# Kernel optimization log

Hardware: AMD Instinct MI355X
Metric: run time of the kernel (lower is better)

The kernel has to match this reference:

```python
import jax, jax.numpy as jnp
import numpy as np
from jax import lax


def setup_inputs() -> dict:
    key = jax.random.key(0)
    k1, k2 = jax.random.split(key)
    B, H, W, C = 8, 32, 32, 512
    N = 16384
    feature_batch = jax.random.normal(k1, (B, H, W, C), dtype=jnp.float32)
    mb = jax.random.normal(k2, (N, C), dtype=jnp.float32)
    return {"feature_batch": feature_batch, "mb": mb, "b": 9}


def reference(feature_batch, mb, b):
    B, H, W, C = feature_batch.shape
    fv = feature_batch.reshape(B * H * W, C)                       # (Q, C)
    sq = (
        jnp.sum(fv * fv, axis=1)[:, None]
        + jnp.sum(mb * mb, axis=1)[None, :]
        - 2.0 * (fv @ mb.T)
    )                                                               # (Q, N)
    sq = jnp.maximum(sq, 0.0)  # guard fp round-off before sqrt
    # smallest-b distances, sorted ascending (top_k of negated values)
    neg_topk = lax.top_k(-sq, b)[0]                                 # (Q, b)
    top_k_dists_squared = -neg_topk
    pixel_scores = jnp.sqrt(top_k_dists_squared[:, 0]).reshape(B, H * W)
    max_idx = jnp.argmax(pixel_scores, axis=1)                      # (B,)
    softmax_args = jnp.sqrt(
        top_k_dists_squared.reshape(B, H * W, b)[jnp.arange(B), max_idx, :]
    )                                                               # (B, b)
    image_scores = softmax_args[:, 0]
    if b > 1:
        image_scores = image_scores * (1.0 - jax.nn.softmax(softmax_args, axis=1)[:, 0])
    pixel_scores = pixel_scores.reshape(B, 1, H, W)
    return pixel_scores, image_scores
```

## Files before the change

kernel.cpp:

```cpp
#include <hip/hip_runtime.h>

typedef unsigned short u16;

#define M_ROWS 8192
#define N_ROWS 16384
#define KDIM   512
#define BM     256
#define BN     256
#define BK     32
#define NCHUNKS 16
#define NPER   (N_ROWS / NCHUNKS)
#define TOPK   9

#define ASZ (BM * BK)
#define BSZ (BN * BK)
#define NTT ((NPER / BN) * (KDIM / BK))

typedef __attribute__((ext_vector_type(8)))  short bf16x8;
typedef __attribute__((ext_vector_type(16))) float f32x16;

__device__ __forceinline__ void gload_lds16(const void* g, void* l) {
  __builtin_amdgcn_global_load_lds(
      (const __attribute__((address_space(1))) void*)g,
      (__attribute__((address_space(3))) void*)l,
      16, 0, 0);
}

__device__ __forceinline__ u16 f2bf(float x) {
  union { float f; unsigned u; } c; c.f = x;
  unsigned u = c.u;
  u += 0x7fffu + ((u >> 16) & 1u);
  return (u16)(u >> 16);
}

__device__ __forceinline__ void topk_update(float v, float* best) {
  if (v < best[TOPK - 1]) {
    #pragma unroll
    for (int i = 0; i < TOPK; ++i) {
      float b = best[i];
      best[i] = fminf(b, v);
      v = fmaxf(b, v);
    }
  }
}

__global__ __launch_bounds__(256) void prep_kernel(
    const float* __restrict__ fv, const float* __restrict__ mb,
    u16* __restrict__ fvb, u16* __restrict__ mbb,
    float* __restrict__ nf, float* __restrict__ nm_perm)
{
  int idx = blockIdx.x * 4 + (threadIdx.x >> 6);
  int l = threadIdx.x & 63;
  const float* src; u16* dst;
  if (idx < M_ROWS) {
    src = fv + (size_t)idx * KDIM; dst = fvb + (size_t)idx * KDIM;
  } else {
    int r = idx - M_ROWS;
    src = mb + (size_t)r * KDIM; dst = mbb + (size_t)r * KDIM;
  }
  float4 x0 = ((const float4*)src)[2 * l];
  float4 x1 = ((const float4*)src)[2 * l + 1];
  float s = x0.x * x0.x + x0.y * x0.y + x0.z * x0.z + x0.w * x0.w
          + x1.x * x1.x + x1.y * x1.y + x1.z * x1.z + x1.w * x1.w;
  uint4 o;
  o.x = (unsigned)f2bf(x0.x) | ((unsigned)f2bf(x0.y) << 16);
  o.y = (unsigned)f2bf(x0.z) | ((unsigned)f2bf(x0.w) << 16);
  o.z = (unsigned)f2bf(x1.x) | ((unsigned)f2bf(x1.y) << 16);
  o.w = (unsigned)f2bf(x1.z) | ((unsigned)f2bf(x1.w) << 16);
  ((uint4*)dst)[l] = o;
  #pragma unroll
  for (int off = 32; off > 0; off >>= 1) s += __shfl_down(s, off, 64);
  if (l == 0) {
    if (idx < M_ROWS) {
      nf[idx] = s;
    } else {
      int n  = idx - M_ROWS;
      int ig = n >> 5;
      int w5 = n & 31;
      int h  = (w5 >> 2) & 1;
      int r  = (w5 & 3) | ((w5 >> 3) << 2);
      nm_perm[(ig * 2 + h) * 16 + r] = s;
    }
  }
}

__global__ __launch_bounds__(512, 2) void gemm_topk_kernel(
    const u16* __restrict__ fvb, const u16* __restrict__ mbb,
    const float* __restrict__ nm_perm, float* __restrict__ partial)
{
  extern __shared__ __align__(16) u16 sm[];
  u16* const Asm = sm;
  u16* const Bsm = sm + 3 * ASZ;

  const int t   = threadIdx.x;
  const int l   = t & 63;
  const int w   = t >> 6;
  const int wm  = w >> 1;
  const int wn  = w & 1;
  const int h   = l >> 5;
  const int c31 = l & 31;
  const int xr  = (c31 >> 1) & 3;

  const int m0    = blockIdx.x * BM;
  const int ncoff = blockIdx.y * NPER;

  const int srow = l >> 2;
  const int sc   = ((l & 3) ^ ((l >> 3) & 3)) * 8;

  const u16* aSrc = fvb + (size_t)(m0 + w * 32 + srow) * KDIM + sc;
  const u16* bSrc = mbb + (size_t)(ncoff + w * 32 + srow) * KDIM + sc;

  const int aRd  = (wm * 64 + c31) * BK;
  const int bRd  = (wn * 128 + c31) * BK;
  const int ch0  = (h ^ xr) * 8;
  const int ch1  = ch0 ^ 16;

#define STAGE(tt2_, bufS_) do {                                               \
    const size_t ao_ = (size_t)((tt2_) & 15) * BK;                            \
    const size_t bo_ = (size_t)((tt2_) >> 4) * ((size_t)BN * KDIM) + ao_;     \
    u16* ad_ = Asm + (bufS_) * ASZ + (w * 32) * BK;                           \
    u16* bd_ = Bsm + (bufS_) * BSZ + (w * 32) * BK;                           \
    gload_lds16(aSrc + ao_,             ad_);                                 \
    gload_lds16(aSrc + ao_ + 16 * KDIM, ad_ + 16 * BK);                       \
    gload_lds16(bSrc + bo_,             bd_);                                 \
    gload_lds16(bSrc + bo_ + 16 * KDIM, bd_ + 16 * BK);                       \
  } while (0)

  float best[2][TOPK];
  float T[2];
  #pragma unroll
  for (int s = 0; s < 2; ++s) {
    T[s] = 3.4e38f;
    #pragma unroll
    for (int i = 0; i < TOPK; ++i) best[s][i] = 3.4e38f;
  }

  f32x16 acc[2][4];

  STAGE(0, 0);
  STAGE(1, 1);
  asm volatile("s_waitcnt vmcnt(4)" ::: "memory");
  __builtin_amdgcn_s_barrier();

  int bC = 0, bS = 2;
  for (int tt = 0; tt < NTT; ++tt) {
    if ((tt & 15) == 0) {
      #pragma unroll
      for (int s = 0; s < 2; ++s)
        #pragma unroll
        for (int i = 0; i < 4; ++i)
          #pragma unroll
          for (int r = 0; r < 16; ++r) acc[s][i][r] = 0.0f;
    }

    if (tt + 2 < NTT) STAGE(tt + 2, bS);

    {
      const u16* Ak = Asm + bC * ASZ;
      const u16* Bk = Bsm + bC * BSZ;
      {
        bf16x8 f0 = *(const bf16x8*)&Ak[aRd + ch0];
        bf16x8 f1 = *(const bf16x8*)&Ak[aRd + 32 * BK + ch0];
        #pragma unroll
        for (int i = 0; i < 4; ++i) {
          bf16x8 mbf = *(const bf16x8*)&Bk[bRd + i * 32 * BK + ch0];
          acc[0][i] = __builtin_amdgcn_mfma_f32_32x32x16_bf16(mbf, f0, acc[0][i], 0, 0, 0);
          acc[1][i] = __builtin_amdgcn_mfma_f32_32x32x16_bf16(mbf, f1, acc[1][i], 0, 0, 0);
        }
      }
      {
        bf16x8 f0 = *(const bf16x8*)&Ak[aRd + ch1];
        bf16x8 f1 = *(const bf16x8*)&Ak[aRd + 32 * BK + ch1];
        #pragma unroll
        for (int i = 0; i < 4; ++i) {
          bf16x8 mbf = *(const bf16x8*)&Bk[bRd + i * 32 * BK + ch1];
          acc[0][i] = __builtin_amdgcn_mfma_f32_32x32x16_bf16(mbf, f0, acc[0][i], 0, 0, 0);
          acc[1][i] = __builtin_amdgcn_mfma_f32_32x32x16_bf16(mbf, f1, acc[1][i], 0, 0, 0);
        }
      }
    }

    if (tt < NTT - 1) {
      if (tt < NTT - 2) { asm volatile("s_waitcnt vmcnt(4)" ::: "memory"); }
      else              { asm volatile("s_waitcnt vmcnt(0)" ::: "memory"); }
      __builtin_amdgcn_s_barrier();
    }

    if ((tt & 15) == 15) {
      const int nt    = tt >> 4;
      const int nbase = ncoff + nt * BN;
      #pragma unroll
      for (int i = 0; i < 4; ++i) {
        const float4* np =
            (const float4*)&nm_perm[(((nbase >> 5) + wn * 4 + i) * 2 + h) * 16];
        float4 q0 = np[0], q1 = np[1], q2 = np[2], q3 = np[3];
        #pragma unroll
        for (int s = 0; s < 2; ++s) {
          float v[16];
          v[ 0] = fmaf(-2.0f, acc[s][i][ 0], q0.x);
          v[ 1] = fmaf(-2.0f, acc[s][i][ 1], q0.y);
          v[ 2] = fmaf(-2.0f, acc[s][i][ 2], q0.z);
          v[ 3] = fmaf(-2.0f, acc[s][i][ 3], q0.w);
          v[ 4] = fmaf(-2.0f, acc[s][i][ 4], q1.x);
          v[ 5] = fmaf(-2.0f, acc[s][i][ 5], q1.y);
          v[ 6] = fmaf(-2.0f, acc[s][i][ 6], q1.z);
          v[ 7] = fmaf(-2.0f, acc[s][i][ 7], q1.w);
          v[ 8] = fmaf(-2.0f, acc[s][i][ 8], q2.x);
          v[ 9] = fmaf(-2.0f, acc[s][i][ 9], q2.y);
          v[10] = fmaf(-2.0f, acc[s][i][10], q2.z);
          v[11] = fmaf(-2.0f, acc[s][i][11], q2.w);
          v[12] = fmaf(-2.0f, acc[s][i][12], q3.x);
          v[13] = fmaf(-2.0f, acc[s][i][13], q3.y);
          v[14] = fmaf(-2.0f, acc[s][i][14], q3.z);
          v[15] = fmaf(-2.0f, acc[s][i][15], q3.w);
          float bmin = 3.4e38f;
          #pragma unroll
          for (int r = 0; r < 16; ++r) bmin = fminf(bmin, v[r]);
          if (bmin < T[s]) {
            #pragma unroll
            for (int r = 0; r < 16; ++r) topk_update(v[r], best[s]);
            T[s] = best[s][TOPK - 1];
          }
        }
      }
      #pragma unroll
      for (int s = 0; s < 2; ++s)
        T[s] = fminf(best[s][TOPK - 1], __shfl_xor(best[s][TOPK - 1], 32, 64));
    }

    bC = (bC == 2) ? 0 : bC + 1;
    bS = (bS == 2) ? 0 : bS + 1;
  }

  #pragma unroll
  for (int s = 0; s < 2; ++s) {
    float tmp[TOPK];
    #pragma unroll
    for (int q = 0; q < TOPK; ++q) tmp[q] = __shfl_xor(best[s][q], 32, 64);
    #pragma unroll
    for (int q = 0; q < TOPK; ++q) topk_update(tmp[q], best[s]);
  }

  float* smerge = (float*)sm;
  __syncthreads();
  if (wn == 1 && h == 0) {
    #pragma unroll
    for (int s = 0; s < 2; ++s)
      #pragma unroll
      for (int q = 0; q < TOPK; ++q)
        smerge[(wm * 64 + s * 32 + c31) * TOPK + q] = best[s][q];
  }
  __syncthreads();
  if (wn == 0) {
    #pragma unroll
    for (int s = 0; s < 2; ++s) {
      const float* p = &smerge[(wm * 64 + s * 32 + c31) * TOPK];
      #pragma unroll
      for (int q = 0; q < TOPK; ++q) topk_update(p[q], best[s]);
      int m = m0 + wm * 64 + s * 32 + c31;
      size_t base = ((size_t)blockIdx.y * M_ROWS + m) * TOPK;
      if (h == 0) {
        #pragma unroll
        for (int q = 0; q < 5; ++q) partial[base + q] = best[s][q];
      } else {
        #pragma unroll
        for (int q = 5; q < TOPK; ++q) partial[base + q] = best[s][q];
      }
    }
  }
}

__global__ __launch_bounds__(256) void merge_kernel(
    const float* __restrict__ partial, const float* __restrict__ nf,
    float* __restrict__ final9, float* __restrict__ out_pix)
{
  int row = blockIdx.x * 256 + threadIdx.x;
  float best[TOPK];
  #pragma unroll
  for (int i = 0; i < TOPK; ++i) best[i] = 3.4e38f;
  for (int s = 0; s < NCHUNKS; ++s) {
    const float* p = &partial[((size_t)s * M_ROWS + row) * TOPK];
    #pragma unroll
    for (int i = 0; i < TOPK; ++i) topk_update(p[i], best);
  }
  float nfr = nf[row];
  float d[TOPK];
  #pragma unroll
  for (int i = 0; i < TOPK; ++i) d[i] = sqrtf(fmaxf(best[i] + nfr, 0.0f));
  out_pix[row] = d[0];
  #pragma unroll
  for (int i = 0; i < TOPK; ++i) final9[(size_t)row * TOPK + i] = d[i];
}

__global__ __launch_bounds__(256) void img_kernel(
    const float* __restrict__ out_pix, const float* __restrict__ final9,
    const int* __restrict__ bptr, float* __restrict__ out_img)
{
  int img = blockIdx.x, t = threadIdx.x;
  float bv = -1.0f; int bi = 0;
  for (int p = t; p < 1024; p += 256) {
    float v = out_pix[img * 1024 + p];
    if (v > bv) { bv = v; bi = p; }
  }
  __shared__ float sv[256];
  __shared__ int   si[256];
  sv[t] = bv; si[t] = bi;
  __syncthreads();
  for (int off = 128; off > 0; off >>= 1) {
    if (t < off) {
      float v2 = sv[t + off]; int i2 = si[t + off];
      if (v2 > sv[t] || (v2 == sv[t] && i2 < si[t])) { sv[t] = v2; si[t] = i2; }
    }
    __syncthreads();
  }
  if (t == 0) {
    int row = img * 1024 + si[0];
    int b = bptr[0];
    float s0 = final9[(size_t)row * TOPK + 0];
    float score = s0;
    if (b > 1) {
      int bb = b < TOPK ? b : TOPK;
      float mx = s0;
      for (int i = 1; i < bb; ++i) mx = fmaxf(mx, final9[(size_t)row * TOPK + i]);
      float den = 0.0f;
      for (int i = 0; i < bb; ++i) den += expf(final9[(size_t)row * TOPK + i] - mx);
      score = s0 * (1.0f - expf(s0 - mx) / den);
    }
    out_img[img] = score;
  }
}

extern "C" void kernel_launch(void* const* d_in, const int* in_sizes, int n_in,
                              void* d_out, int out_size, void* d_ws, size_t ws_size,
                              hipStream_t stream) {
  const float* fv   = (const float*)d_in[0];
  const float* mb   = (const float*)d_in[1];
  const int*   bptr = (const int*)d_in[2];
  float* out = (float*)d_out;

  char* ws = (char*)d_ws;
  u16*   fvb     = (u16*)ws;
  u16*   mbb     = (u16*)(ws + 8388608);
  float* nf      = (float*)(ws + 25165824);
  float* nm_perm = (float*)(ws + 25198592);
  float* partial = (float*)(ws + 25264128);
  float* final9  = (float*)(ws + 29982720);

  hipLaunchKernelGGL(prep_kernel, dim3((M_ROWS + N_ROWS) / 4), dim3(256), 0, stream,
                     fv, mb, fvb, mbb, nf, nm_perm);
  hipLaunchKernelGGL(gemm_topk_kernel, dim3(M_ROWS / BM, NCHUNKS), dim3(512),
                     98304, stream, fvb, mbb, nm_perm, partial);
  hipLaunchKernelGGL(merge_kernel, dim3(M_ROWS / 256), dim3(256), 0, stream,
                     partial, nf, final9, out);
  hipLaunchKernelGGL(img_kernel, dim3(8), dim3(256), 0, stream,
                     out, final9, bptr, out + M_ROWS);
}
```

Measured before the change: 344.7 us.

## Split K-step into two phases interleaving A/B staging with MFMA and halve chunks

The main loop now preloads all LDS fragments for each half of the BK step, issues the A (then B) global-to-LDS prefetch between the LDS reads and the MFMAs, and raises wave priority around the MFMA clusters, with extra barriers to keep waves in lockstep. The N dimension is split into 8 chunks instead of 16, so there are fewer blocks, each doing longer work, and fewer partial top-k results to merge. The workspace offset for the final buffer moves to match the smaller partial array. The aim is to overlap global loads with matrix math and cut merge traffic. The cost is extra barriers per iteration and a grid of only 256 blocks, which may leave compute units underfilled.

```diff
diff --git a/kernel.cpp b/kernel.cpp
--- a/kernel.cpp
+++ b/kernel.cpp
@@ -8,7 +8,7 @@
 #define BM     256
 #define BN     256
 #define BK     32
-#define NCHUNKS 16
+#define NCHUNKS 8
 #define NPER   (N_ROWS / NCHUNKS)
 #define TOPK   9
 
@@ -115,13 +115,16 @@
   const int ch0  = (h ^ xr) * 8;
   const int ch1  = ch0 ^ 16;
 
-#define STAGE(tt2_, bufS_) do {                                               \
+#define STAGE_A(tt2_, bufS_) do {                                             \
     const size_t ao_ = (size_t)((tt2_) & 15) * BK;                            \
-    const size_t bo_ = (size_t)((tt2_) >> 4) * ((size_t)BN * KDIM) + ao_;     \
     u16* ad_ = Asm + (bufS_) * ASZ + (w * 32) * BK;                           \
-    u16* bd_ = Bsm + (bufS_) * BSZ + (w * 32) * BK;                           \
     gload_lds16(aSrc + ao_,             ad_);                                 \
     gload_lds16(aSrc + ao_ + 16 * KDIM, ad_ + 16 * BK);                       \
+  } while (0)
+#define STAGE_B(tt2_, bufS_) do {                                             \
+    const size_t bo_ = (size_t)((tt2_) >> 4) * ((size_t)BN * KDIM)            \
+                     + (size_t)((tt2_) & 15) * BK;                            \
+    u16* bd_ = Bsm + (bufS_) * BSZ + (w * 32) * BK;                           \
     gload_lds16(bSrc + bo_,             bd_);                                 \
     gload_lds16(bSrc + bo_ + 16 * KDIM, bd_ + 16 * BK);                       \
   } while (0)
@@ -137,8 +140,8 @@
 
   f32x16 acc[2][4];
 
-  STAGE(0, 0);
-  STAGE(1, 1);
+  STAGE_A(0, 0); STAGE_B(0, 0);
+  STAGE_A(1, 1); STAGE_B(1, 1);
   asm volatile("s_waitcnt vmcnt(4)" ::: "memory");
   __builtin_amdgcn_s_barrier();
 
@@ -153,37 +156,58 @@
           for (int r = 0; r < 16; ++r) acc[s][i][r] = 0.0f;
     }
 
-    if (tt + 2 < NTT) STAGE(tt + 2, bS);
+    const u16* Ak = Asm + bC * ASZ;
+    const u16* Bk = Bsm + bC * BSZ;
+    const bool doStage = (tt + 2 < NTT);
 
     {
-      const u16* Ak = Asm + bC * ASZ;
-      const u16* Bk = Bsm + bC * BSZ;
-      {
-        bf16x8 f0 = *(const bf16x8*)&Ak[aRd + ch0];
-        bf16x8 f1 = *(const bf16x8*)&Ak[aRd + 32 * BK + ch0];
-        #pragma unroll
-        for (int i = 0; i < 4; ++i) {
-          bf16x8 mbf = *(const bf16x8*)&Bk[bRd + i * 32 * BK + ch0];
-          acc[0][i] = __builtin_amdgcn_mfma_f32_32x32x16_bf16(mbf, f0, acc[0][i], 0, 0, 0);
-          acc[1][i] = __builtin_amdgcn_mfma_f32_32x32x16_bf16(mbf, f1, acc[1][i], 0, 0, 0);
-        }
+      bf16x8 f0 = *(const bf16x8*)&Ak[aRd + ch0];
+      bf16x8 f1 = *(const bf16x8*)&Ak[aRd + 32 * BK + ch0];
+      bf16x8 g0 = *(const bf16x8*)&Bk[bRd + 0 * 32 * BK + ch0];
+      bf16x8 g1 = *(const bf16x8*)&Bk[bRd + 1 * 32 * BK + ch0];
+      bf16x8 g2 = *(const bf16x8*)&Bk[bRd + 2 * 32 * BK + ch0];
+      bf16x8 g3 = *(const bf16x8*)&Bk[bRd + 3 * 32 * BK + ch0];
+      if (doStage) STAGE_A(tt + 2, bS);
+      __builtin_amdgcn_s_barrier();
+      asm volatile("s_waitcnt lgkmcnt(0)" ::: "memory");
+      __builtin_amdgcn_s_setprio(1);
+      acc[0][0] = __builtin_amdgcn_mfma_f32_32x32x16_bf16(g0, f0, acc[0][0], 0, 0, 0);
+      acc[1][0] = __builtin_amdgcn_mfma_f32_32x32x16_bf16(g0, f1, acc[1][0], 0, 0, 0);
+      acc[0][1] = __builtin_amdgcn_mfma_f32_32x32x16_bf16(g1, f0, acc[0][1], 0, 0, 0);
+      acc[1][1] = __builtin_amdgcn_mfma_f32_32x32x16_bf16(g1, f1, acc[1][1], 0, 0, 0);
+      acc[0][2] = __builtin_amdgcn_mfma_f32_32x32x16_bf16(g2, f0, acc[0][2], 0, 0, 0);
+      acc[1][2] = __builtin_amdgcn_mfma_f32_32x32x16_bf16(g2, f1, acc[1][2], 0, 0, 0);
+      acc[0][3] = __builtin_amdgcn_mfma_f32_32x32x16_bf16(g3, f0, acc[0][3], 0, 0, 0);
+      acc[1][3] = __builtin_amdgcn_mfma_f32_32x32x16_bf16(g3, f1, acc[1][3], 0, 0, 0);
+      __builtin_amdgcn_s_setprio(0);
+      __builtin_amdgcn_s_barrier();
+    }
+
+    {
+      bf16x8 f0 = *(const bf16x8*)&Ak[aRd + ch1];
+      bf16x8 f1 = *(const bf16x8*)&Ak[aRd + 32 * BK + ch1];
+      bf16x8 g0 = *(const bf16x8*)&Bk[bRd + 0 * 32 * BK + ch1];
+      bf16x8 g1 = *(const bf16x8*)&Bk[bRd + 1 * 32 * BK + ch1];
+      bf16x8 g2 = *(const bf16x8*)&Bk[bRd + 2 * 32 * BK + ch1];
+      bf16x8 g3 = *(const bf16x8*)&Bk[bRd + 3 * 32 * BK + ch1];
+      if (doStage) STAGE_B(tt + 2, bS);
+      __builtin_amdgcn_s_barrier();
+      asm volatile("s_waitcnt lgkmcnt(0)" ::: "memory");
+      __builtin_amdgcn_s_setprio(1);
+      acc[0][0] = __builtin_amdgcn_mfma_f32_32x32x16_bf16(g0, f0, acc[0][0], 0, 0, 0);
+      acc[1][0] = __builtin_amdgcn_mfma_f32_32x32x16_bf16(g0, f1, acc[1][0], 0, 0, 0);
+      acc[0][1] = __builtin_amdgcn_mfma_f32_32x32x16_bf16(g1, f0, acc[0][1], 0, 0, 0);
+      acc[1][1] = __builtin_amdgcn_mfma_f32_32x32x16_bf16(g1, f1, acc[1][1], 0, 0, 0);
+      acc[0][2] = __builtin_amdgcn_mfma_f32_32x32x16_bf16(g2, f0, acc[0][2], 0, 0, 0);
+      acc[1][2] = __builtin_amdgcn_mfma_f32_32x32x16_bf16(g2, f1, acc[1][2], 0, 0, 0);
+      acc[0][3] = __builtin_amdgcn_mfma_f32_32x32x16_bf16(g3, f0, acc[0][3], 0, 0, 0);
+      acc[1][3] = __builtin_amdgcn_mfma_f32_32x32x16_bf16(g3, f1, acc[1][3], 0, 0, 0);
+      __builtin_amdgcn_s_setprio(0);
+      if (tt < NTT - 1) {
+        if (tt < NTT - 2) { asm volatile("s_waitcnt vmcnt(4)" ::: "memory"); }
+        else              { asm volatile("s_waitcnt vmcnt(0)" ::: "memory"); }
+        __builtin_amdgcn_s_barrier();
       }
-      {
-        bf16x8 f0 = *(const bf16x8*)&Ak[aRd + ch1];
-        bf16x8 f1 = *(const bf16x8*)&Ak[aRd + 32 * BK + ch1];
-        #pragma unroll
-        for (int i = 0; i < 4; ++i) {
-          bf16x8 mbf = *(const bf16x8*)&Bk[bRd + i * 32 * BK + ch1];
-          acc[0][i] = __builtin_amdgcn_mfma_f32_32x32x16_bf16(mbf, f0, acc[0][i], 0, 0, 0);
-          acc[1][i] = __builtin_amdgcn_mfma_f32_32x32x16_bf16(mbf, f1, acc[1][i], 0, 0, 0);
-        }
-      }
-    }
-
-    if (tt < NTT - 1) {
-      if (tt < NTT - 2) { asm volatile("s_waitcnt vmcnt(4)" ::: "memory"); }
-      else              { asm volatile("s_waitcnt vmcnt(0)" ::: "memory"); }
-      __builtin_amdgcn_s_barrier();
     }
 
     if ((tt & 15) == 15) {
@@ -344,7 +368,7 @@
   float* nf      = (float*)(ws + 25165824);
   float* nm_perm = (float*)(ws + 25198592);
   float* partial = (float*)(ws + 25264128);
-  float* final9  = (float*)(ws + 29982720);
+  float* final9  = (float*)(ws + 27623424);
 
   hipLaunchKernelGGL(prep_kernel, dim3((M_ROWS + N_ROWS) / 4), dim3(256), 0, stream,
                      fv, mb, fvb, mbb, nf, nm_perm);
```

Result: no change. 341.4 us (-1.0%).
